# Performance work log

Hardware: AMD Instinct MI355X
Metric: run time of the kernel (lower is better)

Reference implementation:

```python
import jax, jax.numpy as jnp
import numpy as np
from jax import lax

# Matches init_kwargs: ops='co', window_size=[51, 25]
OPS = "co"
WINDOWS = [51, 25]


def _stage(x, k, mode):
    # Torch Conv1d(padding='same') zero-pads left=(k-1)//2, right=k//2, and the
    # identity-shift kernel bank + channel min/max is exactly a sliding-window
    # min/max over the zero-padded signal.
    left, right = (k - 1) // 2, k // 2
    xp = jnp.pad(x, ((0, 0), (0, 0), (left, right)))  # zeros, as in torch 'same'
    if mode == "max":  # dilation
        return lax.reduce_window(xp, float("-inf"), lax.max, (1, 1, k), (1, 1, 1), "VALID")
    # erosion
    return lax.reduce_window(xp, float("inf"), lax.min, (1, 1, k), (1, 1, 1), "VALID")


def _chain(x):
    # Per-channel python loop in the original is channel-independent; we batch it.
    for op, k in zip(OPS, WINDOWS):
        if op.lower() == "c":  # closing: dilation then erosion
            x = _stage(x, k, "max")
            x = _stage(x, k, "min")
        elif op.lower() == "o":  # opening: erosion then dilation
            x = _stage(x, k, "min")
            x = _stage(x, k, "max")
    return x


def setup_inputs() -> dict:
    key = jax.random.key(0)
    x = jax.random.normal(key, (16, 8, 262144), dtype=jnp.float32)  # [B, C, L]
    return {"x": x}


def reference(x):
    return _chain(x)
```

## Files before the change

### kernel.cpp

```cpp
#include <hip/hip_runtime.h>


#define L_ROW   262144
#define N_ROWS  128
#define BLOCK   256
#define E       32
#define EF4     8
#define T_W     1880
#define N_CHUNKS 140
#define NSLOT   512

typedef float f32x2 __attribute__((ext_vector_type(2)));

__device__ __forceinline__ int swz(int s) { return s ^ ((s >> 3) & 7); }

#define WFENCE() asm volatile("" ::: "memory")

template<bool MX>
__device__ __forceinline__ float mm(float a, float b) {
  return MX ? fmaxf(a, b) : fminf(a, b);
}

__device__ __forceinline__ void edge_zero(float* r, int goff, int lane, bool edge) {
  if (edge) {
    const int base = goff + lane * E;
#pragma unroll
    for (int i = 0; i < E; ++i)
      if ((unsigned)(base + i) >= (unsigned)L_ROW) r[i] = 0.0f;
  }
}

__device__ __forceinline__ void writeback(const float* r, float4* buf, int b4) {
  WFENCE();
#pragma unroll
  for (int j = 0; j < EF4; ++j)
    buf[swz(b4 + j)] = make_float4(r[4*j], r[4*j+1], r[4*j+2], r[4*j+3]);
  WFENCE();
}

template<int K, bool MX>
__device__ __forceinline__ void stage_big(float* r, float4* buf, int lane,
                                          int goff, bool edge) {
  constexpr int BLEN = K - 33;
  constexpr int BN   = (BLEN + 2) / 4;
  const int b4 = lane * EF4;
  const int bh = min(b4, NSLOT - 16 - BN);

  float4 v0 = buf[swz(bh + 8)];
  float a0 = v0.x, a1 = v0.y, a2 = v0.z, a3 = v0.w;
#pragma unroll
  for (int j = 1; j < BN - 1; ++j) {
    float4 v = buf[swz(bh + 8 + j)];
    a0 = mm<MX>(a0, v.x); a1 = mm<MX>(a1, v.y);
    a2 = mm<MX>(a2, v.z); a3 = mm<MX>(a3, v.w);
  }
  float4 vl = buf[swz(bh + 8 + BN - 1)];
  const float Base = mm<MX>(mm<MX>(mm<MX>(a0, a1), mm<MX>(a2, a3)),
                            mm<MX>(vl.x, vl.y));
  float T[34];
  T[0] = vl.z; T[1] = vl.w;
#pragma unroll
  for (int j = 0; j < 8; ++j) {
    float4 v = buf[swz(bh + 8 + BN + j)];
    T[2+4*j] = v.x; T[3+4*j] = v.y; T[4+4*j] = v.z; T[5+4*j] = v.w;
  }

#pragma unroll
  for (int b = 0; b < 4; ++b)
#pragma unroll
    for (int i = 8*b + 6; i >= 8*b; --i) r[i] = mm<MX>(r[i], r[i+1]);
  const float S2 = r[24];
  const float S1 = mm<MX>(r[16], S2);
  const float S0 = mm<MX>(r[8],  S1);
#pragma unroll
  for (int i = 0;  i < 8;  ++i) r[i] = mm<MX>(r[i], S0);
#pragma unroll
  for (int i = 8;  i < 16; ++i) r[i] = mm<MX>(r[i], S1);
#pragma unroll
  for (int i = 16; i < 24; ++i) r[i] = mm<MX>(r[i], S2);

#pragma unroll
  for (int b = 0; b < 4; ++b)
#pragma unroll
    for (int i = 8*b + 1; i < 8*b + 8; ++i) T[i] = mm<MX>(T[i-1], T[i]);
  const float G0 = mm<MX>(Base, T[7]);
  const float G1 = mm<MX>(G0,   T[15]);
  const float G2 = mm<MX>(G1,   T[23]);

#pragma unroll
  for (int i = 0;  i < 8;  ++i) r[i] = mm<MX>(r[i], mm<MX>(Base, T[i]));
#pragma unroll
  for (int i = 8;  i < 16; ++i) r[i] = mm<MX>(r[i], mm<MX>(G0, T[i]));
#pragma unroll
  for (int i = 16; i < 24; ++i) r[i] = mm<MX>(r[i], mm<MX>(G1, T[i]));
#pragma unroll
  for (int i = 24; i < 32; ++i) r[i] = mm<MX>(r[i], mm<MX>(G2, T[i]));

  edge_zero(r, goff, lane, edge);
  writeback(r, buf, b4);
}

template<bool MX>
__device__ __forceinline__ void stage_25(float* r, float4* buf, int lane,
                                         int goff, bool edge) {
  const int b4 = lane * EF4;
  const int bh = min(b4, NSLOT - 14);
  float h[24];
#pragma unroll
  for (int j = 0; j < 6; ++j) {
    float4 v = buf[swz(bh + 8 + j)];
    h[4*j] = v.x; h[4*j+1] = v.y; h[4*j+2] = v.z; h[4*j+3] = v.w;
  }

  float t[8];
  t[0] = r[24];
#pragma unroll
  for (int i = 1; i < 8; ++i) t[i] = mm<MX>(t[i-1], r[24+i]);
#pragma unroll
  for (int i = 30; i >= 24; --i) r[i] = mm<MX>(r[i], r[i+1]);
#pragma unroll
  for (int i = 22; i >= 16; --i) r[i] = mm<MX>(r[i], r[i+1]);
  const float cA = r[16];
  const float A3 = r[24];
#pragma unroll
  for (int i = 16; i < 24; ++i) r[i] = mm<MX>(r[i], A3);
#pragma unroll
  for (int i = 14; i >= 8; --i) r[i] = mm<MX>(r[i], r[i+1]);
#pragma unroll
  for (int i = 6;  i >= 0; --i) r[i] = mm<MX>(r[i], r[i+1]);
  const float A1 = r[8];
#pragma unroll
  for (int i = 0; i < 8; ++i) r[i] = mm<MX>(r[i], A1);
#pragma unroll
  for (int b = 0; b < 3; ++b)
#pragma unroll
    for (int i = 8*b + 1; i < 8*b + 8; ++i) h[i] = mm<MX>(h[i-1], h[i]);
  const float aB  = h[7];
  const float cA2 = mm<MX>(cA, t[7]);
  const float G1  = mm<MX>(aB, h[15]);
#pragma unroll
  for (int i = 0;  i < 8;  ++i) r[i] = mm<MX>(r[i], mm<MX>(cA,  t[i]));
#pragma unroll
  for (int i = 8;  i < 16; ++i) r[i] = mm<MX>(r[i], mm<MX>(cA2, h[i-8]));
#pragma unroll
  for (int i = 16; i < 24; ++i) r[i] = mm<MX>(r[i], mm<MX>(aB,  h[i-8]));
#pragma unroll
  for (int i = 24; i < 32; ++i) r[i] = mm<MX>(r[i], mm<MX>(G1,  h[i-8]));

  edge_zero(r, goff, lane, edge);
  writeback(r, buf, b4);
}

__global__ __launch_bounds__(BLOCK)
void morph_co_kernel(const float* __restrict__ x, float* __restrict__ out) {
  __shared__ float4 lds4[4 * NSLOT];

  const int w    = threadIdx.x >> 6;
  const int lane = threadIdx.x & 63;
  const int c    = blockIdx.x * 4 + w;
  const int row  = blockIdx.y;

  float4* buf = lds4 + w * NSLOT;
  const float* __restrict__ xrow = x   + (size_t)row * L_ROW;
  float* __restrict__       orow = out + (size_t)row * L_ROW;

  const int ob = c * T_W;
  const int c0 = ob - 76;
  const bool edge = (c == 0) || (c == N_CHUNKS - 1);
  const int b4 = lane * EF4;
  float r[E];

  if (!edge) {
#pragma unroll
    for (int it = 0; it < 8; ++it) {
      const int s = it * 64 + lane;
      const float* g = xrow + c0 + 4 * swz(s);
      __builtin_amdgcn_global_load_lds(
          (const __attribute__((address_space(1))) void*)g,
          (__attribute__((address_space(3))) void*)(&buf[it * 64]), 16, 0, 0);
    }
    asm volatile("s_waitcnt vmcnt(0)" ::: "memory");
  } else {
#pragma unroll
    for (int it = 0; it < 8; ++it) {
      const int s = it * 64 + lane;
      const int g = c0 + 4 * s;
      float4 v;
      v.x = ((unsigned)(g + 0) < (unsigned)L_ROW) ? xrow[g + 0] : 0.0f;
      v.y = ((unsigned)(g + 1) < (unsigned)L_ROW) ? xrow[g + 1] : 0.0f;
      v.z = ((unsigned)(g + 2) < (unsigned)L_ROW) ? xrow[g + 2] : 0.0f;
      v.w = ((unsigned)(g + 3) < (unsigned)L_ROW) ? xrow[g + 3] : 0.0f;
      buf[swz(s)] = v;
    }
    WFENCE();
  }

#pragma unroll
  for (int j = 0; j < EF4; ++j) {
    float4 v = buf[swz(b4 + j)];
    r[4*j] = v.x; r[4*j+1] = v.y; r[4*j+2] = v.z; r[4*j+3] = v.w;
  }

  if (!edge) {
    stage_big<51, true >(r, buf, lane, 0, false);
    stage_big<75, false>(r, buf, lane, 0, false);
    stage_25 <true >(r, buf, lane, 0, false);
  } else {
    stage_big<51, true >(r, buf, lane, c0 + 25, true);
    stage_big<51, false>(r, buf, lane, c0 + 50, true);
    stage_25 <false>(r, buf, lane, c0 + 62, true);
    stage_25 <true >(r, buf, lane, c0 + 74, true);
  }

  if (!edge) {
#pragma unroll
    for (int it = 0; it < 8; ++it) {
      const int u = it * 64 + lane;
      if (u <= T_W / 4) {
        float4 v = buf[swz(u)];
        float* p = orow + ob + 4 * u;
        if (u >= 1)          *reinterpret_cast<f32x2*>(p - 2) = f32x2{v.x, v.y};
        if (u <  T_W / 4)    *reinterpret_cast<f32x2*>(p)     = f32x2{v.z, v.w};
      }
    }
  } else {
    const int hi = min(ob + T_W, L_ROW);
#pragma unroll
    for (int it = 0; it < 8; ++it) {
      const int u = it * 64 + lane;
      if (u <= T_W / 4) {
        float4 v = buf[swz(u)];
        const int p = ob - 2 + 4 * u;
        if (p     >= ob && p     < hi) orow[p]     = v.x;
        if (p + 1 >= ob && p + 1 < hi) orow[p + 1] = v.y;
        if (p + 2 >= ob && p + 2 < hi) orow[p + 2] = v.z;
        if (p + 3 >= ob && p + 3 < hi) orow[p + 3] = v.w;
      }
    }
  }
}

extern "C" void kernel_launch(void* const* d_in, const int* in_sizes, int n_in,
                              void* d_out, int out_size, void* d_ws, size_t ws_size,
                              hipStream_t stream) {
  const float* x = (const float*)d_in[0];
  float* out = (float*)d_out;
  dim3 grid(N_CHUNKS / 4, N_ROWS);
  morph_co_kernel<<<grid, BLOCK, 0, stream>>>(x, out);
}
```

Baseline: 49.57 us.

## Process four chunks per single-wave block with register prefetch of next chunk

Each block is now one 64-lane wave that walks four consecutive chunks in sequence. It replaces the earlier four independent waves per block, each handling one chunk. While the current chunk is computed, the next chunk's input is loaded into registers and later stored to LDS. The aim is to hide global load latency behind the min/max stages. The direct global-to-LDS async load is dropped in favour of a register round trip. Serialising chunks within a wave cuts the number of waves in flight, so per-wave latency hiding may be weaker, and the prefetch buffer raises register use.

```diff
diff --git a/kernel.cpp b/kernel.cpp
--- a/kernel.cpp
+++ b/kernel.cpp
@@ -3,11 +3,13 @@
 
 #define L_ROW   262144
 #define N_ROWS  128
-#define BLOCK   256
+#define BLOCK   64
+#define CPW     4
 #define E       32
 #define EF4     8
 #define T_W     1880
 #define N_CHUNKS 140
+#define N_TASKS 35
 #define NSLOT   512
 
 typedef float f32x2 __attribute__((ext_vector_type(2)));
@@ -153,88 +155,103 @@
 
 __global__ __launch_bounds__(BLOCK)
 void morph_co_kernel(const float* __restrict__ x, float* __restrict__ out) {
-  __shared__ float4 lds4[4 * NSLOT];
-
-  const int w    = threadIdx.x >> 6;
-  const int lane = threadIdx.x & 63;
-  const int c    = blockIdx.x * 4 + w;
+  __shared__ float4 buf[NSLOT];
+
+  const int lane = threadIdx.x;
   const int row  = blockIdx.y;
-
-  float4* buf = lds4 + w * NSLOT;
+  const int c_base = blockIdx.x * CPW;
+
   const float* __restrict__ xrow = x   + (size_t)row * L_ROW;
   float* __restrict__       orow = out + (size_t)row * L_ROW;
-
-  const int ob = c * T_W;
-  const int c0 = ob - 76;
-  const bool edge = (c == 0) || (c == N_CHUNKS - 1);
   const int b4 = lane * EF4;
-  float r[E];
-
-  if (!edge) {
-#pragma unroll
-    for (int it = 0; it < 8; ++it) {
-      const int s = it * 64 + lane;
-      const float* g = xrow + c0 + 4 * swz(s);
-      __builtin_amdgcn_global_load_lds(
-          (const __attribute__((address_space(1))) void*)g,
-          (__attribute__((address_space(3))) void*)(&buf[it * 64]), 16, 0, 0);
-    }
-    asm volatile("s_waitcnt vmcnt(0)" ::: "memory");
-  } else {
-#pragma unroll
-    for (int it = 0; it < 8; ++it) {
-      const int s = it * 64 + lane;
-      const int g = c0 + 4 * s;
-      float4 v;
-      v.x = ((unsigned)(g + 0) < (unsigned)L_ROW) ? xrow[g + 0] : 0.0f;
-      v.y = ((unsigned)(g + 1) < (unsigned)L_ROW) ? xrow[g + 1] : 0.0f;
-      v.z = ((unsigned)(g + 2) < (unsigned)L_ROW) ? xrow[g + 2] : 0.0f;
-      v.w = ((unsigned)(g + 3) < (unsigned)L_ROW) ? xrow[g + 3] : 0.0f;
-      buf[swz(s)] = v;
-    }
-    WFENCE();
-  }
-
-#pragma unroll
-  for (int j = 0; j < EF4; ++j) {
-    float4 v = buf[swz(b4 + j)];
-    r[4*j] = v.x; r[4*j+1] = v.y; r[4*j+2] = v.z; r[4*j+3] = v.w;
-  }
-
-  if (!edge) {
-    stage_big<51, true >(r, buf, lane, 0, false);
-    stage_big<75, false>(r, buf, lane, 0, false);
-    stage_25 <true >(r, buf, lane, 0, false);
-  } else {
-    stage_big<51, true >(r, buf, lane, c0 + 25, true);
-    stage_big<51, false>(r, buf, lane, c0 + 50, true);
-    stage_25 <false>(r, buf, lane, c0 + 62, true);
-    stage_25 <true >(r, buf, lane, c0 + 74, true);
-  }
-
-  if (!edge) {
-#pragma unroll
-    for (int it = 0; it < 8; ++it) {
-      const int u = it * 64 + lane;
-      if (u <= T_W / 4) {
-        float4 v = buf[swz(u)];
-        float* p = orow + ob + 4 * u;
-        if (u >= 1)          *reinterpret_cast<f32x2*>(p - 2) = f32x2{v.x, v.y};
-        if (u <  T_W / 4)    *reinterpret_cast<f32x2*>(p)     = f32x2{v.z, v.w};
+
+  float4 pv[8];
+
+  if (c_base != 0) {
+    const int c0p = c_base * T_W - 76;
+#pragma unroll
+    for (int it = 0; it < 8; ++it)
+      pv[it] = *reinterpret_cast<const float4*>(
+          xrow + c0p + 4 * swz(it * 64 + lane));
+  }
+
+  for (int k = 0; k < CPW; ++k) {
+    const int c  = c_base + k;
+    const int ob = c * T_W;
+    const int c0 = ob - 76;
+    const bool edge = (c == 0) || (c == N_CHUNKS - 1);
+
+    if (edge) {
+#pragma unroll
+      for (int it = 0; it < 8; ++it) {
+        const int s = it * 64 + lane;
+        const int g = c0 + 4 * s;
+        float4 v;
+        v.x = ((unsigned)(g + 0) < (unsigned)L_ROW) ? xrow[g + 0] : 0.0f;
+        v.y = ((unsigned)(g + 1) < (unsigned)L_ROW) ? xrow[g + 1] : 0.0f;
+        v.z = ((unsigned)(g + 2) < (unsigned)L_ROW) ? xrow[g + 2] : 0.0f;
+        v.w = ((unsigned)(g + 3) < (unsigned)L_ROW) ? xrow[g + 3] : 0.0f;
+        buf[swz(s)] = v;
       }
-    }
-  } else {
-    const int hi = min(ob + T_W, L_ROW);
-#pragma unroll
-    for (int it = 0; it < 8; ++it) {
-      const int u = it * 64 + lane;
-      if (u <= T_W / 4) {
-        float4 v = buf[swz(u)];
-        const int p = ob - 2 + 4 * u;
-        if (p     >= ob && p     < hi) orow[p]     = v.x;
-        if (p + 1 >= ob && p + 1 < hi) orow[p + 1] = v.y;
-        if (p + 2 >= ob && p + 2 < hi) orow[p + 2] = v.z;
-        if (p + 3 >= ob && p + 3 < hi) orow[p + 3] = v.w;
+      WFENCE();
+    } else {
+      WFENCE();
+#pragma unroll
+      for (int it = 0; it < 8; ++it)
+        buf[it * 64 + lane] = pv[it];
+      WFENCE();
+    }
+
+    if (k < CPW - 1 && (c + 1) != N_CHUNKS - 1) {
+      const int c0n = (c + 1) * T_W - 76;
+#pragma unroll
+      for (int it = 0; it < 8; ++it)
+        pv[it] = *reinterpret_cast<const float4*>(
+            xrow + c0n + 4 * swz(it * 64 + lane));
+    }
+
+    float r[E];
+#pragma unroll
+    for (int j = 0; j < EF4; ++j) {
+      float4 v = buf[swz(b4 + j)];
+      r[4*j] = v.x; r[4*j+1] = v.y; r[4*j+2] = v.z; r[4*j+3] = v.w;
+    }
+
+    if (!edge) {
+      stage_big<51, true >(r, buf, lane, 0, false);
+      stage_big<75, false>(r, buf, lane, 0, false);
+      stage_25 <true >(r, buf, lane, 0, false);
+    } else {
+      stage_big<51, true >(r, buf, lane, c0 + 25, true);
+      stage_big<51, false>(r, buf, lane, c0 + 50, true);
+      stage_25 <false>(r, buf, lane, c0 + 62, true);
+      stage_25 <true >(r, buf, lane, c0 + 74, true);
+    }
+
+    if (!edge) {
+#pragma unroll
+      for (int it = 0; it < 8; ++it) {
+        const int u = it * 64 + lane;
+        if (u <= T_W / 4) {
+          float4 v = buf[swz(u)];
+          float* p = orow + ob + 4 * u;
+          if (u >= 1)       *reinterpret_cast<f32x2*>(p - 2) = f32x2{v.x, v.y};
+          if (u < T_W / 4)  *reinterpret_cast<f32x2*>(p)     = f32x2{v.z, v.w};
+        }
+      }
+    } else {
+      const int hi = min(ob + T_W, L_ROW);
+#pragma unroll
+      for (int it = 0; it < 8; ++it) {
+        const int u = it * 64 + lane;
+        if (u <= T_W / 4) {
+          float4 v = buf[swz(u)];
+          const int p = ob - 2 + 4 * u;
+          if (p     >= ob && p     < hi) orow[p]     = v.x;
+          if (p + 1 >= ob && p + 1 < hi) orow[p + 1] = v.y;
+          if (p + 2 >= ob && p + 2 < hi) orow[p + 2] = v.z;
+          if (p + 3 >= ob && p + 3 < hi) orow[p + 3] = v.w;
+        }
       }
     }
   }
@@ -245,6 +262,6 @@
                               hipStream_t stream) {
   const float* x = (const float*)d_in[0];
   float* out = (float*)d_out;
-  dim3 grid(N_CHUNKS / 4, N_ROWS);
+  dim3 grid(N_TASKS, N_ROWS);
   morph_co_kernel<<<grid, BLOCK, 0, stream>>>(x, out);
 }
```

Result: slower. 146.5 us (+195.6%).

## Process two chunks per wave with prefetch of second chunk overlapping first compute

Applied to the files above, without the earlier changes.

Each wave now handles two consecutive chunks. It issues the async global-to-LDS loads for both up front, then waits only for the first chunk's loads (vmcnt(8)) before computing it, so the second chunk's load overlaps the first chunk's compute. The block shrinks to 128 threads with the same 4 chunks per block. This cuts the number of waves and exposes memory latency less, but each wave's work is serialized and there is less parallelism from wave count. The edge-chunk handling relies on chunk 0 always landing in slot A and the last chunk in slot B.

```diff
diff --git a/kernel.cpp b/kernel.cpp
--- a/kernel.cpp
+++ b/kernel.cpp
@@ -3,7 +3,7 @@
 
 #define L_ROW   262144
 #define N_ROWS  128
-#define BLOCK   256
+#define BLOCK   128
 #define E       32
 #define EF4     8
 #define T_W     1880
@@ -151,50 +151,44 @@
   writeback(r, buf, b4);
 }
 
-__global__ __launch_bounds__(BLOCK)
-void morph_co_kernel(const float* __restrict__ x, float* __restrict__ out) {
-  __shared__ float4 lds4[4 * NSLOT];
-
-  const int w    = threadIdx.x >> 6;
-  const int lane = threadIdx.x & 63;
-  const int c    = blockIdx.x * 4 + w;
-  const int row  = blockIdx.y;
-
-  float4* buf = lds4 + w * NSLOT;
-  const float* __restrict__ xrow = x   + (size_t)row * L_ROW;
-  float* __restrict__       orow = out + (size_t)row * L_ROW;
-
+__device__ __forceinline__ void stage_issue(int c, float4* buf, int lane,
+                                            const float* xrow) {
+  const int c0 = c * T_W - 76;
+#pragma unroll
+  for (int it = 0; it < 8; ++it) {
+    const int s = it * 64 + lane;
+    const float* g = xrow + c0 + 4 * swz(s);
+    __builtin_amdgcn_global_load_lds(
+        (const __attribute__((address_space(1))) void*)g,
+        (__attribute__((address_space(3))) void*)(&buf[it * 64]), 16, 0, 0);
+  }
+}
+
+__device__ __forceinline__ void stage_edge(int c, float4* buf, int lane,
+                                           const float* xrow) {
+  const int c0 = c * T_W - 76;
+#pragma unroll
+  for (int it = 0; it < 8; ++it) {
+    const int s = it * 64 + lane;
+    const int g = c0 + 4 * s;
+    float4 v;
+    v.x = ((unsigned)(g + 0) < (unsigned)L_ROW) ? xrow[g + 0] : 0.0f;
+    v.y = ((unsigned)(g + 1) < (unsigned)L_ROW) ? xrow[g + 1] : 0.0f;
+    v.z = ((unsigned)(g + 2) < (unsigned)L_ROW) ? xrow[g + 2] : 0.0f;
+    v.w = ((unsigned)(g + 3) < (unsigned)L_ROW) ? xrow[g + 3] : 0.0f;
+    buf[swz(s)] = v;
+  }
+  WFENCE();
+}
+
+__device__ __forceinline__ void process_chunk(int c, float4* buf, int lane,
+                                              float* orow) {
   const int ob = c * T_W;
   const int c0 = ob - 76;
   const bool edge = (c == 0) || (c == N_CHUNKS - 1);
   const int b4 = lane * EF4;
+
   float r[E];
-
-  if (!edge) {
-#pragma unroll
-    for (int it = 0; it < 8; ++it) {
-      const int s = it * 64 + lane;
-      const float* g = xrow + c0 + 4 * swz(s);
-      __builtin_amdgcn_global_load_lds(
-          (const __attribute__((address_space(1))) void*)g,
-          (__attribute__((address_space(3))) void*)(&buf[it * 64]), 16, 0, 0);
-    }
-    asm volatile("s_waitcnt vmcnt(0)" ::: "memory");
-  } else {
-#pragma unroll
-    for (int it = 0; it < 8; ++it) {
-      const int s = it * 64 + lane;
-      const int g = c0 + 4 * s;
-      float4 v;
-      v.x = ((unsigned)(g + 0) < (unsigned)L_ROW) ? xrow[g + 0] : 0.0f;
-      v.y = ((unsigned)(g + 1) < (unsigned)L_ROW) ? xrow[g + 1] : 0.0f;
-      v.z = ((unsigned)(g + 2) < (unsigned)L_ROW) ? xrow[g + 2] : 0.0f;
-      v.w = ((unsigned)(g + 3) < (unsigned)L_ROW) ? xrow[g + 3] : 0.0f;
-      buf[swz(s)] = v;
-    }
-    WFENCE();
-  }
-
 #pragma unroll
   for (int j = 0; j < EF4; ++j) {
     float4 v = buf[swz(b4 + j)];
@@ -219,8 +213,8 @@
       if (u <= T_W / 4) {
         float4 v = buf[swz(u)];
         float* p = orow + ob + 4 * u;
-        if (u >= 1)          *reinterpret_cast<f32x2*>(p - 2) = f32x2{v.x, v.y};
-        if (u <  T_W / 4)    *reinterpret_cast<f32x2*>(p)     = f32x2{v.z, v.w};
+        if (u >= 1)       *reinterpret_cast<f32x2*>(p - 2) = f32x2{v.x, v.y};
+        if (u < T_W / 4)  *reinterpret_cast<f32x2*>(p)     = f32x2{v.z, v.w};
       }
     }
   } else {
@@ -240,6 +234,40 @@
   }
 }
 
+__global__ __launch_bounds__(BLOCK)
+void morph_co_kernel(const float* __restrict__ x, float* __restrict__ out) {
+  __shared__ float4 lds4[2 * 2 * NSLOT];
+
+  const int w    = threadIdx.x >> 6;
+  const int lane = threadIdx.x & 63;
+  const int row  = blockIdx.y;
+
+  const float* __restrict__ xrow = x   + (size_t)row * L_ROW;
+  float* __restrict__       orow = out + (size_t)row * L_ROW;
+
+  float4* bufA = lds4 + w * (2 * NSLOT);
+  float4* bufB = bufA + NSLOT;
+
+  const int cA = blockIdx.x * 4 + 2 * w;
+  const int cB = cA + 1;
+  const bool eA = (cA == 0);
+  const bool eB = (cB == N_CHUNKS - 1);
+
+  if (!eA) stage_issue(cA, bufA, lane, xrow);
+  if (!eB) stage_issue(cB, bufB, lane, xrow);
+  if (eA)  stage_edge (cA, bufA, lane, xrow);
+  if (eB)  stage_edge (cB, bufB, lane, xrow);
+
+  if (!eA) {
+    if (eB) { asm volatile("s_waitcnt vmcnt(0)" ::: "memory"); }
+    else    { asm volatile("s_waitcnt vmcnt(8)" ::: "memory"); }
+  }
+  process_chunk(cA, bufA, lane, orow);
+
+  if (!eB) { asm volatile("s_waitcnt vmcnt(0)" ::: "memory"); }
+  process_chunk(cB, bufB, lane, orow);
+}
+
 extern "C" void kernel_launch(void* const* d_in, const int* in_sizes, int n_in,
                               void* d_out, int out_size, void* d_ws, size_t ws_size,
                               hipStream_t stream) {
```

After: 52.78 us. 1.06x slower.
